# Performance work log

Measured on AMD Instinct MI355X. Metric: run time of the kernel, lower is better.

Reference implementation:

```python
import jax, jax.numpy as jnp
import numpy as np

B, C_IN, H, W = 8, 256, 32, 32
DK = 256
DV = 256
NH = 8
DKH = DK // NH  # 32
C_OUT = 512
KS, PAD = 3, 1


def setup_inputs() -> dict:
    key = jax.random.key(0)
    ks = jax.random.split(key, 9)
    s = 0.05
    return {
        "x": jax.random.normal(ks[0], (B, C_IN, H, W), jnp.float32),
        "w_qkv": jax.random.normal(ks[1], (2 * DK + DV, C_IN, 1, 1), jnp.float32) * s,
        "b_qkv": jnp.zeros((2 * DK + DV,), jnp.float32),
        "w_attn": jax.random.normal(ks[2], (DV, DV, 1, 1), jnp.float32) * s,
        "b_attn": jnp.zeros((DV,), jnp.float32),
        "w_out": jax.random.normal(ks[3], (C_OUT - DV, C_IN, KS, KS), jnp.float32) * s,
        "b_out": jnp.zeros((C_OUT - DV,), jnp.float32),
        # torch init: dkh**-0.5 + rand
        "key_rel_w": DKH ** (-0.5) + jax.random.uniform(ks[4], (2 * W - 1, DKH), jnp.float32),
        "key_rel_h": DKH ** (-0.5) + jax.random.uniform(ks[5], (2 * H - 1, DKH), jnp.float32),
    }


def conv2d(x, w, b, pad):
    y = jax.lax.conv_general_dilated(
        x, w, window_strides=(1, 1), padding=[(pad, pad), (pad, pad)],
        dimension_numbers=("NCHW", "OIHW", "NCHW"))
    return y + b[None, :, None, None]


def rel_to_abs(x):
    # x: [b, nh, L, 2L-1] -> [b, nh, L, L] (skew trick)
    b, nh, L, _ = x.shape
    x = jnp.pad(x, ((0, 0), (0, 0), (0, 0), (0, 1)))
    flat = x.reshape(b, nh, L * 2 * L)
    flat = jnp.pad(flat, ((0, 0), (0, 0), (0, L - 1)))
    final = flat.reshape(b, nh, L + 1, 2 * L - 1)
    return final[:, :, :L, L - 1:]


def relative_logits_1d(q, rel_k, Hd, Wd, transpose_mask):
    # q: [B, NH, DKH, Hd, Wd]; rel_k: [2*Wd-1, DKH]
    rel = jnp.einsum("bhdxy,md->bhxym", q, rel_k)          # [B,NH,Hd,Wd,2Wd-1]
    rel = rel.reshape(-1, NH * Hd, Wd, 2 * Wd - 1)
    rel = rel_to_abs(rel)                                   # [B,NH*Hd,Wd,Wd]
    rel = rel.reshape(-1, NH, Hd, 1, Wd, Wd)
    rel = jnp.broadcast_to(rel, (rel.shape[0], NH, Hd, Hd, Wd, Wd))
    rel = jnp.transpose(rel, transpose_mask)
    return rel.reshape(-1, NH, Hd * Wd, Hd * Wd)


def reference(x, w_qkv, b_qkv, w_attn, b_attn, w_out, b_out, key_rel_w, key_rel_h):
    conv_out = conv2d(x, w_out, b_out, PAD)                 # [B, C_OUT-DV, H, W]
    qkv = conv2d(x, w_qkv, b_qkv, 0)                        # [B, 2DK+DV, H, W]
    q, k, v = jnp.split(qkv, [DK, 2 * DK], axis=1)
    q = q.reshape(B, NH, DKH, H * W) * (DKH ** -0.5)        # scaled BEFORE rel logits (as in torch)
    k = k.reshape(B, NH, DKH, H * W)
    v = v.reshape(B, NH, DV // NH, H * W)
    logits = jnp.einsum("bhdl,bhdm->bhlm", q, k)            # [B,NH,HW,HW]
    q5 = q.reshape(B, NH, DKH, H, W)
    w_rel = relative_logits_1d(q5, key_rel_w, H, W, (0, 1, 2, 4, 3, 5))
    h_rel = relative_logits_1d(jnp.transpose(q5, (0, 1, 2, 4, 3)), key_rel_h, W, H, (0, 1, 4, 2, 5, 3))
    logits = logits + h_rel + w_rel
    weights = jax.nn.softmax(logits, axis=-1)
    attn = jnp.einsum("bhlm,bhdm->bhdl", weights, v)        # [B,NH,DVH,HW]
    attn = attn.reshape(B, DV, H, W)
    attn = conv2d(attn, w_attn, b_attn, 0)
    return jnp.concatenate([conv_out, attn], axis=1)        # [B, C_OUT, H, W]
```

## Files before the change

kernel.cpp:

```cpp
#include <hip/hip_runtime.h>
#include <hip/hip_bf16.h>


typedef __hip_bfloat16 bf16;
typedef __attribute__((ext_vector_type(8))) short bf16x8;
typedef __attribute__((ext_vector_type(4))) float f32x4;

__device__ __forceinline__ float blo(unsigned int v) { return __uint_as_float(v << 16); }
__device__ __forceinline__ float bhi(unsigned int v) { return __uint_as_float(v & 0xffff0000u); }
__device__ __forceinline__ unsigned short f2bfbits(float f) {
  union { bf16 h; unsigned short u; } cv; cv.h = __float2bfloat16(f); return cv.u;
}
__device__ __forceinline__ unsigned int cvt_pk_bf16(float lo, float hi) {
  unsigned int r;
  asm("v_cvt_pk_bf16_f32 %0, %1, %2" : "=v"(r) : "v"(lo), "v"(hi));
  return r;
}
__device__ __forceinline__ float exp2_f(float x) {
#if __has_builtin(__builtin_amdgcn_exp2f)
  return __builtin_amdgcn_exp2f(x);
#else
  return exp2f(x);
#endif
}

__global__ __launch_bounds__(256) void prep_kernel(
    const float* __restrict__ x, const float* __restrict__ wout,
    bf16* __restrict__ xT, bf16* __restrict__ wob0, bf16* __restrict__ wob1)
{
  int bid = blockIdx.x, tid = threadIdx.x;
  if (bid < 2048) {
    __shared__ float t[32 * 33];
    int b = bid >> 8, rem = bid & 255;
    int ci0 = (rem >> 5) * 32, l0 = (rem & 31) * 32;
    {
      int ciL = tid >> 3, lL4 = (tid & 7) * 4;
      float4 v = *(const float4*)(x + (size_t)(b * 256 + ci0 + ciL) * 1024 + l0 + lL4);
      t[ciL * 33 + lL4 + 0] = v.x; t[ciL * 33 + lL4 + 1] = v.y;
      t[ciL * 33 + lL4 + 2] = v.z; t[ciL * 33 + lL4 + 3] = v.w;
    }
    __syncthreads();
    {
      int lL = tid >> 3, cS = (tid & 7) * 4;
      unsigned int p0 = (unsigned int)f2bfbits(t[(cS + 0) * 33 + lL]) |
                        ((unsigned int)f2bfbits(t[(cS + 1) * 33 + lL]) << 16);
      unsigned int p1 = (unsigned int)f2bfbits(t[(cS + 2) * 33 + lL]) |
                        ((unsigned int)f2bfbits(t[(cS + 3) * 33 + lL]) << 16);
      uint2 u2; u2.x = p0; u2.y = p1;
      *(uint2*)(xT + ((size_t)(b * 1024) + l0 + lL) * 256 + ci0 + cS) = u2;
    }
  } else {
    int t0 = (bid - 2048) * 256 + tid;
#pragma unroll
    for (int s = 0; s < 8; ++s) {
      int u = s * 9216 + t0;
      int chunkblk = u / 2304;
      int within = u - chunkblk * 2304;
      int co63 = within / 36;
      int r = within - co63 * 36;
      int kidx = r >> 2, cig = r & 3;
      int co = (chunkblk >> 3) * 64 + co63;
      int ci = (chunkblk & 7) * 32 + cig * 8;
      union { unsigned short h[8]; uint4 u4; } pk;
#pragma unroll
      for (int j = 0; j < 8; ++j)
        pk.h[j] = f2bfbits(wout[(size_t)(co * 256 + ci + j) * 9 + kidx]);
      bf16* dst = (chunkblk < 28) ? (wob0 + (size_t)chunkblk * 18432)
                                  : (wob1 + (size_t)(chunkblk - 28) * 18432);
      *(uint4*)(dst + (size_t)within * 8) = pk.u4;
    }
  }
}

__global__ __launch_bounds__(256) void convqkv_kernel(
    const bf16* __restrict__ xT,
    const bf16* __restrict__ wob0, const bf16* __restrict__ wob1,
    const float* __restrict__ b_out, float* __restrict__ out,
    const float* __restrict__ wq, const float* __restrict__ b_qkv,
    bf16* __restrict__ qT, bf16* __restrict__ kR, bf16* __restrict__ vW)
{
  __shared__ __align__(16) short smem[27104];
  int tid = threadIdx.x, lane = tid & 63, wave = tid >> 6;
  int m16 = lane & 15, quad = lane >> 4;

  if (blockIdx.x < 256) {
    short* wS = smem;
    short* xS = smem + 18944;
    int bid = blockIdx.x;
    int rc = bid & 7, cotile = (bid >> 3) & 3, b = bid >> 5;
    int y0 = rc * 4;

    f32x4 acc[8];
#pragma unroll
    for (int t = 0; t < 8; ++t) acc[t] = (f32x4){0.f, 0.f, 0.f, 0.f};

    for (int ck = 0; ck < 8; ++ck) {
      __syncthreads();
      int cb = cotile * 8 + ck;
      const bf16* wbase = (cb < 28) ? (wob0 + (size_t)cb * 18432)
                                    : (wob1 + (size_t)(cb - 28) * 18432);
#pragma unroll
      for (int r = 0; r < 9; ++r) {
        int u = r * 256 + tid;
        *(uint4*)(wS + (u / 36) * 296 + (u % 36) * 8) = *(const uint4*)(wbase + (size_t)u * 8);
      }
#pragma unroll
      for (int r = 0; r < 3; ++r) {
        int u = r * 256 + tid;
        int pos = u >> 2, seg = u & 3;
        int row = pos >> 5, col = pos & 31;
        int gy = y0 - 1 + row;
        uint4 val = make_uint4(0u, 0u, 0u, 0u);
        if (gy >= 0 && gy < 32)
          val = *(const uint4*)(xT + ((size_t)(b * 1024) + gy * 32 + col) * 256 + ck * 32 + seg * 8);
        *(uint4*)(xS + (row * 34 + col + 1) * 40 + seg * 8) = val;
      }
      if (tid < 48) {
        int pos = tid >> 2, seg = tid & 3;
        int row = pos >> 1, side = pos & 1;
        *(uint4*)(xS + (row * 34 + side * 33) * 40 + seg * 8) = make_uint4(0u, 0u, 0u, 0u);
      }
      __syncthreads();
#pragma unroll
      for (int kidx = 0; kidx < 9; ++kidx) {
        int dy = kidx / 3, dx = kidx - dy * 3;
        bf16x8 af = *(const bf16x8*)(wS + (wave * 16 + m16) * 296 + kidx * 32 + quad * 8);
#pragma unroll
        for (int t = 0; t < 8; ++t) {
          int row = (t >> 1) + dy;
          int col = (t & 1) * 16 + m16 + dx;
          bf16x8 bf = *(const bf16x8*)(xS + (row * 34 + col) * 40 + quad * 8);
          acc[t] = __builtin_amdgcn_mfma_f32_16x16x32_bf16(af, bf, acc[t], 0, 0, 0);
        }
      }
    }

    int cob = cotile * 64 + wave * 16 + quad * 4;
#pragma unroll
    for (int i = 0; i < 4; ++i) {
      float bv = b_out[cob + i];
#pragma unroll
      for (int t = 0; t < 8; ++t) {
        int y = y0 + (t >> 1), xc = (t & 1) * 16 + m16;
        out[((size_t)(b * 512) + cob + i) * 1024 + y * 32 + xc] = acc[t][i] + bv;
      }
    }
  } else {
    short* aS = smem;
    short* bS = smem + 4608;
    int bid2 = blockIdx.x - 256;
    int ltile = bid2 & 7;
    int rest = bid2 >> 3;
    int ctile = rest % 12;
    int b = rest / 12;
    int l0 = ltile * 128;
    int cbase = ctile * 64;

    f32x4 acc[8];
#pragma unroll
    for (int t = 0; t < 8; ++t) acc[t] = (f32x4){0.f, 0.f, 0.f, 0.f};

    for (int ck = 0; ck < 4; ++ck) {
      __syncthreads();
#pragma unroll
      for (int r = 0; r < 4; ++r) {
        int u = r * 256 + tid;
        int c = u >> 4, s4 = u & 15;
        float4 v = *(const float4*)(wq + (size_t)(cbase + c) * 256 + ck * 64 + s4 * 4);
        unsigned int p0 = (unsigned int)f2bfbits(v.x) | ((unsigned int)f2bfbits(v.y) << 16);
        unsigned int p1 = (unsigned int)f2bfbits(v.z) | ((unsigned int)f2bfbits(v.w) << 16);
        uint2 u2; u2.x = p0; u2.y = p1;
        *(uint2*)(aS + c * 72 + s4 * 4) = u2;
      }
#pragma unroll
      for (int r = 0; r < 4; ++r) {
        int u = r * 256 + tid;
        int l = u >> 3, seg = u & 7;
        *(uint4*)(bS + l * 72 + seg * 8) =
            *(const uint4*)(xT + ((size_t)(b * 1024) + l0 + l) * 256 + ck * 64 + seg * 8);
      }
      __syncthreads();
#pragma unroll
      for (int ks = 0; ks < 2; ++ks) {
        bf16x8 af = *(const bf16x8*)(aS + (wave * 16 + m16) * 72 + ks * 32 + quad * 8);
#pragma unroll
        for (int t = 0; t < 8; ++t) {
          bf16x8 bf = *(const bf16x8*)(bS + (t * 16 + m16) * 72 + ks * 32 + quad * 8);
          acc[t] = __builtin_amdgcn_mfma_f32_16x16x32_bf16(af, bf, acc[t], 0, 0, 0);
        }
      }
    }

    __syncthreads();
    short* ldsT = smem + wave * 3072;
    int cb = cbase + wave * 16;
    bool isq = (ctile < 4);
    float bv[4];
#pragma unroll
    for (int i = 0; i < 4; ++i) bv[i] = b_qkv[cb + quad * 4 + i];
#pragma unroll
    for (int t = 0; t < 8; ++t) {
#pragma unroll
      for (int i = 0; i < 4; ++i) {
        float v = acc[t][i] + bv[i];
        if (isq) v *= 0.17677669529663689f;
        ldsT[(t * 16 + m16) * 24 + quad * 4 + i] = (short)f2bfbits(v);
      }
    }
    if (ctile < 8) {
      bf16* dst = isq ? qT : kR;
      int coff = isq ? cb : cb - 256;
#pragma unroll
      for (int rep = 0; rep < 4; ++rep) {
        int u = rep * 64 + lane;
        int l = u >> 1, half = u & 1;
        int c0 = coff + half * 8;
        int head = b * 8 + (c0 >> 5), d0 = c0 & 31;
        *(uint4*)(dst + ((size_t)head * 1024 + l0 + l) * 32 + d0) =
            *(const uint4*)(ldsT + l * 24 + half * 8);
      }
    } else {
      int dcol = lane >> 2, lg = lane & 3;
      int c2 = (cb - 512) + dcol;
      int head = b * 8 + (c2 >> 5), gd = c2 & 31;
      int dt = gd >> 4, m16v = gd & 15;
      int cch = ltile * 2 + (lg >> 1);
      int ksv = lg & 1;
      bf16* vbase = vW + (size_t)head * 32768 + cch * 2048 + (dt * 2 + ksv) * 512 + m16v * 8;
#pragma unroll
      for (int s = 0; s < 4; ++s) {
#pragma unroll
        for (int p = 0; p < 4; ++p) {
          int j0 = lg * 32 + s * 8 + p * 2;
          unsigned int u0 = (unsigned short)ldsT[j0 * 24 + dcol];
          unsigned int u1 = (unsigned short)ldsT[(j0 + 1) * 24 + dcol];
          unsigned int w = u0 | (u1 << 16);
          int quadp = (s & 1) * 2 + (p >> 1);
          int jj = (p & 1) * 2 + (s >> 1) * 4;
          *(unsigned int*)(vbase + quadp * 128 + jj) = w;
        }
      }
    }
  }
}

__global__ __launch_bounds__(256) void attn_mfma_kernel(
    const bf16* __restrict__ qT, const bf16* __restrict__ kR, const bf16* __restrict__ vW,
    const float* __restrict__ krw, const float* __restrict__ krh,
    bf16* __restrict__ attL)
{
  __shared__ __align__(16) char smem[34816];
  float* RWf = (float*)smem;
  float* RHf = (float*)(smem + 17408);

  const float L2E = 1.4426950408889634f;

  int tid = threadIdx.x;
  int lane = tid & 63, wave = tid >> 6;
  int m16 = lane & 15, quad = lane >> 4;
  int bid = blockIdx.x;
  int head = ((bid & 7) << 3) | ((bid >> 3) & 7);
  int qt = bid >> 6;
  int row0 = qt * 64;
  int b = head >> 3, h = head & 7;

  {
    int mrow = wave * 16 + m16;
    bool valid = (mrow < 63);
    float4 w0 = make_float4(0.f, 0.f, 0.f, 0.f), w1 = w0, h0 = w0, h1 = w0;
    if (valid) {
      w0 = *(const float4*)(krw + mrow * 32 + quad * 8);
      w1 = *(const float4*)(krw + mrow * 32 + quad * 8 + 4);
      h0 = *(const float4*)(krh + mrow * 32 + quad * 8);
      h1 = *(const float4*)(krh + mrow * 32 + quad * 8 + 4);
    }
    union { unsigned int w[4]; bf16x8 v; } aw, ah;
    aw.w[0] = cvt_pk_bf16(w0.x * L2E, w0.y * L2E);
    aw.w[1] = cvt_pk_bf16(w0.z * L2E, w0.w * L2E);
    aw.w[2] = cvt_pk_bf16(w1.x * L2E, w1.y * L2E);
    aw.w[3] = cvt_pk_bf16(w1.z * L2E, w1.w * L2E);
    ah.w[0] = cvt_pk_bf16(h0.x * L2E, h0.y * L2E);
    ah.w[1] = cvt_pk_bf16(h0.z * L2E, h0.w * L2E);
    ah.w[2] = cvt_pk_bf16(h1.x * L2E, h1.y * L2E);
    ah.w[3] = cvt_pk_bf16(h1.z * L2E, h1.w * L2E);
#pragma unroll
    for (int nt = 0; nt < 4; ++nt) {
      bf16x8 qf = *(const bf16x8*)(
          qT + ((size_t)head * 1024 + row0 + nt * 16 + m16) * 32 + quad * 8);
      f32x4 z = (f32x4){0.f, 0.f, 0.f, 0.f};
      f32x4 dw = __builtin_amdgcn_mfma_f32_16x16x32_bf16(aw.v, qf, z, 0, 0, 0);
      f32x4 dh = __builtin_amdgcn_mfma_f32_16x16x32_bf16(ah.v, qf, z, 0, 0, 0);
#pragma unroll
      for (int i = 0; i < 4; ++i) {
        int mr = wave * 16 + quad * 4 + i;
        RWf[mr * 68 + nt * 16 + m16] = dw[i];
        RHf[mr * 68 + nt * 16 + m16] = dh[i];
      }
    }
  }
  __syncthreads();

  bf16x8 afrag = *(const bf16x8*)(
      qT + ((size_t)head * 1024 + row0 + wave * 16 + m16) * 32 + quad * 8);
  int qloc = wave * 16 + m16;
  int qm = qloc & 31;
  float rwreg[2][4];
#pragma unroll
  for (int par = 0; par < 2; ++par)
#pragma unroll
    for (int i = 0; i < 4; ++i)
      rwreg[par][i] = RWf[(par * 16 + quad * 4 + i - qm + 31) * 68 + qloc];
  int qy = qt * 2 + (qloc >> 5);
  const float* rhp = RHf + (31 - qy) * 68 + qloc;

  const bf16* kp = kR + (size_t)head * 32768 + m16 * 32 + quad * 8;
  const bf16* vp = vW + (size_t)head * 32768 + lane * 8;

  f32x4 oacc[2];
  oacc[0] = (f32x4){0.f, 0.f, 0.f, 0.f};
  oacc[1] = (f32x4){0.f, 0.f, 0.f, 0.f};
  float rsp = 0.f;

#pragma unroll 1
  for (int c = 0; c < 16; ++c) {
    union { uint4 u; bf16x8 v; } kf[4], vf[4];
#pragma unroll
    for (int t = 0; t < 4; ++t)
      kf[t].u = *(const uint4*)(kp + c * 2048 + t * 512);
#pragma unroll
    for (int q = 0; q < 4; ++q)
      vf[q].u = *(const uint4*)(vp + c * 2048 + q * 512);

    float rh0 = rhp[(c * 2 + 0) * 68];
    float rh1 = rhp[(c * 2 + 1) * 68];

    f32x4 sacc[4];
#pragma unroll
    for (int t = 0; t < 4; ++t) {
      f32x4 z = (f32x4){0.f, 0.f, 0.f, 0.f};
      sacc[t] = __builtin_amdgcn_mfma_f32_16x16x32_bf16(kf[t].v, afrag, z, 0, 0, 0);
    }

    unsigned int pk[4][2];
#pragma unroll
    for (int t = 0; t < 4; ++t) {
      float rh = (t < 2) ? rh0 : rh1;
      float e0 = exp2_f(fmaf(sacc[t][0], L2E, rwreg[t & 1][0] + rh));
      float e1 = exp2_f(fmaf(sacc[t][1], L2E, rwreg[t & 1][1] + rh));
      float e2 = exp2_f(fmaf(sacc[t][2], L2E, rwreg[t & 1][2] + rh));
      float e3 = exp2_f(fmaf(sacc[t][3], L2E, rwreg[t & 1][3] + rh));
      rsp += (e0 + e1) + (e2 + e3);
      pk[t][0] = cvt_pk_bf16(e0, e1);
      pk[t][1] = cvt_pk_bf16(e2, e3);
    }

#pragma unroll
    for (int ks = 0; ks < 2; ++ks) {
      union { unsigned int w[4]; bf16x8 v; } pf;
      pf.w[0] = pk[2 * ks][0];     pf.w[1] = pk[2 * ks][1];
      pf.w[2] = pk[2 * ks + 1][0]; pf.w[3] = pk[2 * ks + 1][1];
#pragma unroll
      for (int dt = 0; dt < 2; ++dt) {
        oacc[dt] = __builtin_amdgcn_mfma_f32_16x16x32_bf16(vf[dt * 2 + ks].v, pf.v, oacc[dt], 0, 0, 0);
      }
    }
  }

  rsp += __shfl_xor(rsp, 16, 64);
  rsp += __shfl_xor(rsp, 32, 64);
  float invs = 1.0f / rsp;
  int grow = row0 + wave * 16 + m16;
#pragma unroll
  for (int dt = 0; dt < 2; ++dt) {
    uint2 st;
    st.x = cvt_pk_bf16(oacc[dt][0] * invs, oacc[dt][1] * invs);
    st.y = cvt_pk_bf16(oacc[dt][2] * invs, oacc[dt][3] * invs);
    *(uint2*)(attL + ((size_t)b * 1024 + grow) * 256 + h * 32 + dt * 16 + quad * 4) = st;
  }
}

__global__ __launch_bounds__(256) void attnout_mfma_kernel(
    const bf16* __restrict__ attL, const float* __restrict__ w, const float* __restrict__ bias,
    float* __restrict__ out)
{
  __shared__ __align__(16) short smem[13824];
  short* aS = smem;
  short* bS = smem + 4608;

  int tid = threadIdx.x, lane = tid & 63, wave = tid >> 6;
  int m16 = lane & 15, quad = lane >> 4;
  int l0 = blockIdx.x * 128;
  int cotile = blockIdx.y;
  int b = blockIdx.z;
  int cbase = cotile * 64;

  f32x4 acc[8];
#pragma unroll
  for (int t = 0; t < 8; ++t) acc[t] = (f32x4){0.f, 0.f, 0.f, 0.f};

  for (int ck = 0; ck < 4; ++ck) {
    __syncthreads();
#pragma unroll
    for (int r = 0; r < 4; ++r) {
      int u = r * 256 + tid;
      int c = u >> 4, s4 = u & 15;
      float4 v = *(const float4*)(w + (size_t)(cbase + c) * 256 + ck * 64 + s4 * 4);
      unsigned int p0 = (unsigned int)f2bfbits(v.x) | ((unsigned int)f2bfbits(v.y) << 16);
      unsigned int p1 = (unsigned int)f2bfbits(v.z) | ((unsigned int)f2bfbits(v.w) << 16);
      uint2 u2; u2.x = p0; u2.y = p1;
      *(uint2*)(aS + c * 72 + s4 * 4) = u2;
    }
#pragma unroll
    for (int r = 0; r < 4; ++r) {
      int u = r * 256 + tid;
      int l = u >> 3, seg = u & 7;
      *(uint4*)(bS + l * 72 + seg * 8) =
          *(const uint4*)(attL + ((size_t)(b * 1024) + l0 + l) * 256 + ck * 64 + seg * 8);
    }
    __syncthreads();
#pragma unroll
    for (int ks = 0; ks < 2; ++ks) {
      bf16x8 af = *(const bf16x8*)(aS + (wave * 16 + m16) * 72 + ks * 32 + quad * 8);
#pragma unroll
      for (int t = 0; t < 8; ++t) {
        bf16x8 bf = *(const bf16x8*)(bS + (t * 16 + m16) * 72 + ks * 32 + quad * 8);
        acc[t] = __builtin_amdgcn_mfma_f32_16x16x32_bf16(af, bf, acc[t], 0, 0, 0);
      }
    }
  }

  int co = cbase + wave * 16 + quad * 4;
#pragma unroll
  for (int i = 0; i < 4; ++i) {
    float bv = bias[co + i];
    size_t obase = ((size_t)(b * 512) + 256 + co + i) * 1024 + l0;
#pragma unroll
    for (int t = 0; t < 8; ++t)
      out[obase + t * 16 + m16] = acc[t][i] + bv;
  }
}

extern "C" void kernel_launch(void* const* d_in, const int* in_sizes, int n_in,
                              void* d_out, int out_size, void* d_ws, size_t ws_size,
                              hipStream_t stream) {
  const float* x      = (const float*)d_in[0];
  const float* w_qkv  = (const float*)d_in[1];
  const float* b_qkv  = (const float*)d_in[2];
  const float* w_attn = (const float*)d_in[3];
  const float* b_attn = (const float*)d_in[4];
  const float* w_out  = (const float*)d_in[5];
  const float* b_out  = (const float*)d_in[6];
  const float* krw    = (const float*)d_in[7];
  const float* krh    = (const float*)d_in[8];
  float* out = (float*)d_out;

  bf16* ws    = (bf16*)d_ws;
  bf16* xT    = ws;
  bf16* attL  = ws;
  bf16* qT    = ws + 2097152;
  bf16* kR    = ws + 4194304;
  bf16* vF    = ws + 6291456;

  bf16* wob0 = (bf16*)(out + (size_t)(0 * 512 + 256) * 1024);
  bf16* wob1 = (bf16*)(out + (size_t)(1 * 512 + 256) * 1024);

  prep_kernel<<<dim3(2084), 256, 0, stream>>>(x, w_out, xT, wob0, wob1);
  convqkv_kernel<<<dim3(1024), 256, 0, stream>>>(xT, wob0, wob1, b_out, out,
                                                 w_qkv, b_qkv, qT, kR, vF);
  attn_mfma_kernel<<<dim3(1024), 256, 0, stream>>>(qT, kR, vF, krw, krh, attL);
  attnout_mfma_kernel<<<dim3(8, 4, 8), 256, 0, stream>>>(attL, w_attn, b_attn, out);
}
```

Measured before the change: 145.0 us.

## Process two query subtiles per wave in attention to reuse K/V fragments

Attention blocks shrink from four waves to two, and each wave now handles two 16-row query subtiles. The K and V fragments loaded from global memory are reused for both subtiles, which halves per-block K/V load traffic. The cost is more registers per wave, fewer waves per block, and less latency hiding per CU.

```diff
diff --git a/kernel.cpp b/kernel.cpp
--- a/kernel.cpp
+++ b/kernel.cpp
@@ -244,7 +244,7 @@
   }
 }
 
-__global__ __launch_bounds__(256) void attn_mfma_kernel(
+__global__ __launch_bounds__(128) void attn_mfma_kernel(
     const bf16* __restrict__ qT, const bf16* __restrict__ kR, const bf16* __restrict__ vW,
     const float* __restrict__ krw, const float* __restrict__ krh,
     bf16* __restrict__ attL)
@@ -264,8 +264,10 @@
   int row0 = qt * 64;
   int b = head >> 3, h = head & 7;
 
-  {
-    int mrow = wave * 16 + m16;
+#pragma unroll
+  for (int mt = 0; mt < 2; ++mt) {
+    int mtile = wave * 2 + mt;
+    int mrow = mtile * 16 + m16;
     bool valid = (mrow < 63);
     float4 w0 = make_float4(0.f, 0.f, 0.f, 0.f), w1 = w0, h0 = w0, h1 = w0;
     if (valid) {
@@ -292,7 +294,7 @@
       f32x4 dh = __builtin_amdgcn_mfma_f32_16x16x32_bf16(ah.v, qf, z, 0, 0, 0);
 #pragma unroll
       for (int i = 0; i < 4; ++i) {
-        int mr = wave * 16 + quad * 4 + i;
+        int mr = mtile * 16 + quad * 4 + i;
         RWf[mr * 68 + nt * 16 + m16] = dw[i];
         RHf[mr * 68 + nt * 16 + m16] = dh[i];
       }
@@ -300,26 +302,35 @@
   }
   __syncthreads();
 
-  bf16x8 afrag = *(const bf16x8*)(
-      qT + ((size_t)head * 1024 + row0 + wave * 16 + m16) * 32 + quad * 8);
-  int qloc = wave * 16 + m16;
-  int qm = qloc & 31;
-  float rwreg[2][4];
-#pragma unroll
-  for (int par = 0; par < 2; ++par)
-#pragma unroll
-    for (int i = 0; i < 4; ++i)
-      rwreg[par][i] = RWf[(par * 16 + quad * 4 + i - qm + 31) * 68 + qloc];
-  int qy = qt * 2 + (qloc >> 5);
-  const float* rhp = RHf + (31 - qy) * 68 + qloc;
+  bf16x8 afrag[2];
+  float rwreg[2][2][4];
+  int qloc0 = wave * 32 + m16;
+#pragma unroll
+  for (int sub = 0; sub < 2; ++sub) {
+    int qloc = qloc0 + sub * 16;
+    afrag[sub] = *(const bf16x8*)(
+        qT + ((size_t)head * 1024 + row0 + qloc) * 32 + quad * 8);
+    int qm = qloc & 31;
+#pragma unroll
+    for (int par = 0; par < 2; ++par)
+#pragma unroll
+      for (int i = 0; i < 4; ++i)
+        rwreg[sub][par][i] = RWf[(par * 16 + quad * 4 + i - qm + 31) * 68 + qloc];
+  }
+  int qy = qt * 2 + wave;
+  const float* rhp0 = RHf + (31 - qy) * 68 + qloc0;
+  const float* rhp1 = rhp0 + 16;
 
   const bf16* kp = kR + (size_t)head * 32768 + m16 * 32 + quad * 8;
   const bf16* vp = vW + (size_t)head * 32768 + lane * 8;
 
-  f32x4 oacc[2];
-  oacc[0] = (f32x4){0.f, 0.f, 0.f, 0.f};
-  oacc[1] = (f32x4){0.f, 0.f, 0.f, 0.f};
-  float rsp = 0.f;
+  f32x4 oacc[2][2];
+#pragma unroll
+  for (int sub = 0; sub < 2; ++sub) {
+    oacc[sub][0] = (f32x4){0.f, 0.f, 0.f, 0.f};
+    oacc[sub][1] = (f32x4){0.f, 0.f, 0.f, 0.f};
+  }
+  float rsp[2] = {0.f, 0.f};
 
 #pragma unroll 1
   for (int c = 0; c < 16; ++c) {
@@ -331,51 +342,64 @@
     for (int q = 0; q < 4; ++q)
       vf[q].u = *(const uint4*)(vp + c * 2048 + q * 512);
 
-    float rh0 = rhp[(c * 2 + 0) * 68];
-    float rh1 = rhp[(c * 2 + 1) * 68];
-
-    f32x4 sacc[4];
+    float rh[2][2];
+    rh[0][0] = rhp0[(c * 2 + 0) * 68];  rh[0][1] = rhp0[(c * 2 + 1) * 68];
+    rh[1][0] = rhp1[(c * 2 + 0) * 68];  rh[1][1] = rhp1[(c * 2 + 1) * 68];
+
+    f32x4 sacc[2][4];
 #pragma unroll
     for (int t = 0; t < 4; ++t) {
       f32x4 z = (f32x4){0.f, 0.f, 0.f, 0.f};
-      sacc[t] = __builtin_amdgcn_mfma_f32_16x16x32_bf16(kf[t].v, afrag, z, 0, 0, 0);
-    }
-
-    unsigned int pk[4][2];
-#pragma unroll
-    for (int t = 0; t < 4; ++t) {
-      float rh = (t < 2) ? rh0 : rh1;
-      float e0 = exp2_f(fmaf(sacc[t][0], L2E, rwreg[t & 1][0] + rh));
-      float e1 = exp2_f(fmaf(sacc[t][1], L2E, rwreg[t & 1][1] + rh));
-      float e2 = exp2_f(fmaf(sacc[t][2], L2E, rwreg[t & 1][2] + rh));
-      float e3 = exp2_f(fmaf(sacc[t][3], L2E, rwreg[t & 1][3] + rh));
-      rsp += (e0 + e1) + (e2 + e3);
-      pk[t][0] = cvt_pk_bf16(e0, e1);
-      pk[t][1] = cvt_pk_bf16(e2, e3);
+#pragma unroll
+      for (int sub = 0; sub < 2; ++sub)
+        sacc[sub][t] = __builtin_amdgcn_mfma_f32_16x16x32_bf16(kf[t].v, afrag[sub], z, 0, 0, 0);
+    }
+
+    unsigned int pk[2][4][2];
+#pragma unroll
+    for (int sub = 0; sub < 2; ++sub) {
+#pragma unroll
+      for (int t = 0; t < 4; ++t) {
+        float rhv = rh[sub][t >> 1];
+        float e0 = exp2_f(fmaf(sacc[sub][t][0], L2E, rwreg[sub][t & 1][0] + rhv));
+        float e1 = exp2_f(fmaf(sacc[sub][t][1], L2E, rwreg[sub][t & 1][1] + rhv));
+        float e2 = exp2_f(fmaf(sacc[sub][t][2], L2E, rwreg[sub][t & 1][2] + rhv));
+        float e3 = exp2_f(fmaf(sacc[sub][t][3], L2E, rwreg[sub][t & 1][3] + rhv));
+        rsp[sub] += (e0 + e1) + (e2 + e3);
+        pk[sub][t][0] = cvt_pk_bf16(e0, e1);
+        pk[sub][t][1] = cvt_pk_bf16(e2, e3);
+      }
     }
 
 #pragma unroll
     for (int ks = 0; ks < 2; ++ks) {
-      union { unsigned int w[4]; bf16x8 v; } pf;
-      pf.w[0] = pk[2 * ks][0];     pf.w[1] = pk[2 * ks][1];
-      pf.w[2] = pk[2 * ks + 1][0]; pf.w[3] = pk[2 * ks + 1][1];
-#pragma unroll
-      for (int dt = 0; dt < 2; ++dt) {
-        oacc[dt] = __builtin_amdgcn_mfma_f32_16x16x32_bf16(vf[dt * 2 + ks].v, pf.v, oacc[dt], 0, 0, 0);
-      }
-    }
-  }
-
-  rsp += __shfl_xor(rsp, 16, 64);
-  rsp += __shfl_xor(rsp, 32, 64);
-  float invs = 1.0f / rsp;
-  int grow = row0 + wave * 16 + m16;
-#pragma unroll
-  for (int dt = 0; dt < 2; ++dt) {
-    uint2 st;
-    st.x = cvt_pk_bf16(oacc[dt][0] * invs, oacc[dt][1] * invs);
-    st.y = cvt_pk_bf16(oacc[dt][2] * invs, oacc[dt][3] * invs);
-    *(uint2*)(attL + ((size_t)b * 1024 + grow) * 256 + h * 32 + dt * 16 + quad * 4) = st;
+#pragma unroll
+      for (int sub = 0; sub < 2; ++sub) {
+        union { unsigned int w[4]; bf16x8 v; } pf;
+        pf.w[0] = pk[sub][2 * ks][0];     pf.w[1] = pk[sub][2 * ks][1];
+        pf.w[2] = pk[sub][2 * ks + 1][0]; pf.w[3] = pk[sub][2 * ks + 1][1];
+#pragma unroll
+        for (int dt = 0; dt < 2; ++dt) {
+          oacc[sub][dt] = __builtin_amdgcn_mfma_f32_16x16x32_bf16(
+              vf[dt * 2 + ks].v, pf.v, oacc[sub][dt], 0, 0, 0);
+        }
+      }
+    }
+  }
+
+#pragma unroll
+  for (int sub = 0; sub < 2; ++sub) {
+    rsp[sub] += __shfl_xor(rsp[sub], 16, 64);
+    rsp[sub] += __shfl_xor(rsp[sub], 32, 64);
+    float invs = 1.0f / rsp[sub];
+    int grow = row0 + qloc0 + sub * 16;
+#pragma unroll
+    for (int dt = 0; dt < 2; ++dt) {
+      uint2 st;
+      st.x = cvt_pk_bf16(oacc[sub][dt][0] * invs, oacc[sub][dt][1] * invs);
+      st.y = cvt_pk_bf16(oacc[sub][dt][2] * invs, oacc[sub][dt][3] * invs);
+      *(uint2*)(attL + ((size_t)b * 1024 + grow) * 256 + h * 32 + dt * 16 + quad * 4) = st;
+    }
   }
 }
 
@@ -467,6 +491,6 @@
   prep_kernel<<<dim3(2084), 256, 0, stream>>>(x, w_out, xT, wob0, wob1);
   convqkv_kernel<<<dim3(1024), 256, 0, stream>>>(xT, wob0, wob1, b_out, out,
                                                  w_qkv, b_qkv, qT, kR, vF);
-  attn_mfma_kernel<<<dim3(1024), 256, 0, stream>>>(qT, kR, vF, krw, krh, attL);
+  attn_mfma_kernel<<<dim3(1024), 128, 0, stream>>>(qT, kR, vF, krw, krh, attL);
   attnout_mfma_kernel<<<dim3(8, 4, 8), 256, 0, stream>>>(attL, w_attn, b_attn, out);
 }
```

After: 138.5 us. 4.5% less time.
